# Performance work log

Measured on AMD Instinct MI355X. Metric: run time of the kernel, lower is better.

## Reference

```python
import jax, jax.numpy as jnp
import numpy as np

B = 131072          # batch
T = 1024            # num_task_types
D = 1029            # input_dim = 5 + T  (4 scalar feats + contention effect + T one-hot)
H1, H2 = 64, 32     # hidden_dims


def setup_inputs() -> dict:
    key = jax.random.key(0)
    ks = jax.random.split(key, 8)
    x = jax.random.normal(ks[0], (B, D), dtype=jnp.float32)
    contention = jax.random.normal(ks[1], (T, T), dtype=jnp.float32) * 0.1
    # MLP params (Linear uses y = x @ W.T + b in torch; we store W as (in, out))
    w1 = jax.random.normal(ks[2], (D, H1), dtype=jnp.float32) * (1.0 / np.sqrt(D))
    b1 = jnp.zeros((H1,), dtype=jnp.float32)
    w2 = jax.random.normal(ks[3], (H1, H2), dtype=jnp.float32) * (1.0 / np.sqrt(H1))
    b2 = jnp.zeros((H2,), dtype=jnp.float32)
    w3 = jax.random.normal(ks[4], (H2, 1), dtype=jnp.float32) * (1.0 / np.sqrt(H2))
    b3 = jnp.zeros((1,), dtype=jnp.float32)
    return {"x": x, "contention": contention,
            "w1": w1, "b1": b1, "w2": w2, "b2": b2, "w3": w3, "b3": b3}


def reference(x, contention, w1, b1, w2, b2, w3, b3):
    feats = x[:, :4]                          # density, recent_latency, diversity, time_since_same
    density = x[:, 0:1]                       # (B, 1)
    task_onehot = x[:, 4:4 + T]               # (B, T)
    task_id = jnp.argmax(task_onehot, axis=1) # (B,) int
    # vectorized replacement of the per-sample python loop:
    # gather row, mean over columns, scale by density
    contention_effect = jnp.mean(contention[task_id], axis=1, keepdims=True) * density  # (B, 1)
    combined = jnp.concatenate([feats, contention_effect, task_onehot], axis=1)  # (B, 5+T) == (B, D)
    # MLP (dropout is identity in eval mode)
    h = jax.nn.relu(combined @ w1 + b1)
    h = jax.nn.relu(h @ w2 + b2)
    latency = jax.nn.relu(h @ w3 + b3)        # (B, 1)
    return latency[:, 0]                      # squeeze -> (B,)
```

## Files before the change

kernel.cpp:

```cpp
#include <hip/hip_runtime.h>

typedef __bf16 bf16x8 __attribute__((ext_vector_type(8)));
typedef float f32x4 __attribute__((ext_vector_type(4)));

#define TM 16
#define ROW_F 1029
#define NKB 33
#define LDS_STRIDE 1064

__global__ __launch_bounds__(256) void k_rowmean(const float* __restrict__ cont,
                                                 float* __restrict__ rowmean) {
    __shared__ float red[4];
    int row = blockIdx.x;
    const float4* cr = (const float4*)(cont + (size_t)row * 1024);
    float4 v = cr[threadIdx.x];
    float p = v.x + v.y + v.z + v.w;
    for (int m = 1; m < 64; m <<= 1) p += __shfl_xor(p, m, 64);
    int lane = threadIdx.x & 63, wid = threadIdx.x >> 6;
    if (lane == 0) red[wid] = p;
    __syncthreads();
    if (threadIdx.x == 0)
        rowmean[row] = (red[0] + red[1] + red[2] + red[3]) * (1.0f / 1024.0f);
}

__global__ __launch_bounds__(256) void k_wpack(const float* __restrict__ w1,
                                               __bf16* __restrict__ wfrag) {
    int o = blockIdx.x * 256 + threadIdx.x;
    int j    = o & 7;
    int lane = (o >> 3) & 63;
    int nt   = (o >> 9) & 3;
    int kb   = o >> 11;
    int k = kb * 32 + ((lane >> 4) << 3) + j;
    int n = nt * 16 + (lane & 15);
    float val = 0.0f;
    if (k < 4)          val = w1[k * 64 + n];
    else if (k < 1028)  val = w1[(k + 1) * 64 + n];
    wfrag[o] = (__bf16)val;
}

__global__ __launch_bounds__(256) void k_main(const float* __restrict__ x,
                                              const float* __restrict__ w1,
                                              const float* __restrict__ b1,
                                              const float* __restrict__ w2,
                                              const float* __restrict__ b2,
                                              const float* __restrict__ w3,
                                              const float* __restrict__ b3,
                                              const float* __restrict__ rowmean,
                                              const __bf16* __restrict__ wfrag,
                                              float* __restrict__ out) {
    __shared__ __align__(16) unsigned short x_lds[TM * LDS_STRIDE];
    __shared__ float h1_lds[TM * 65];
    __shared__ float ce_lds[TM];

    const int tid  = threadIdx.x;
    const int lane = tid & 63;
    const int w    = tid >> 6;

    const float4* xt = (const float4*)(x + (size_t)blockIdx.x * (TM * ROW_F));
    for (int i = tid; i < (TM * ROW_F) / 4; i += 256) {
        float4 v = xt[i];
        unsigned e = 4u * (unsigned)i;
        unsigned row = e / ROW_F;
        unsigned col = e - row * ROW_F;
        float vv[4] = {v.x, v.y, v.z, v.w};
        #pragma unroll
        for (int jj = 0; jj < 4; ++jj) {
            unsigned c = col + jj, r = row;
            if (c >= ROW_F) { c -= ROW_F; r += 1; }
            x_lds[r * LDS_STRIDE + c] = __builtin_bit_cast(unsigned short, (__bf16)vv[jj]);
        }
    }
    for (int i = tid; i < TM * (LDS_STRIDE - ROW_F); i += 256) {
        int r = i / (LDS_STRIDE - ROW_F);
        int c = ROW_F + (i - r * (LDS_STRIDE - ROW_F));
        x_lds[r * LDS_STRIDE + c] = 0;
    }
    __syncthreads();

    for (int q = 0; q < 4; ++q) {
        int row = w * 4 + q;
        const unsigned short* rp = &x_lds[row * LDS_STRIDE + 4 + lane * 16];
        float best = -1e30f; int bidx = 4;
        #pragma unroll
        for (int u = 0; u < 4; ++u) {
            ushort4 s4 = *(const ushort4*)(rp + 4 * u);
            unsigned short ss[4] = {s4.x, s4.y, s4.z, s4.w};
            #pragma unroll
            for (int jj = 0; jj < 4; ++jj) {
                float fv = __uint_as_float((unsigned)ss[jj] << 16);
                int c = 4 + lane * 16 + 4 * u + jj;
                if (fv > best) { best = fv; bidx = c; }
            }
        }
        for (int m = 1; m < 64; m <<= 1) {
            float ov = __shfl_xor(best, m, 64);
            int   oi = __shfl_xor(bidx, m, 64);
            if (ov > best || (ov == best && oi < bidx)) { best = ov; bidx = oi; }
        }
        if (lane == 0) {
            float density = __uint_as_float((unsigned)x_lds[row * LDS_STRIDE] << 16);
            ce_lds[row] = rowmean[bidx - 4] * density;
        }
    }
    __syncthreads();

    f32x4 acc = {0.f, 0.f, 0.f, 0.f};
    const float4* wfp = (const float4*)wfrag;
    const unsigned short* abase = &x_lds[(lane & 15) * LDS_STRIDE + ((lane >> 4) << 3)];
    for (int kb = 0; kb < NKB; ++kb) {
        bf16x8 af = *(const bf16x8*)(abase + kb * 32);
        float4 braw = wfp[(kb * 4 + w) * 64 + lane];
        bf16x8 bf = __builtin_bit_cast(bf16x8, braw);
        acc = __builtin_amdgcn_mfma_f32_16x16x32_bf16(af, bf, acc, 0, 0, 0);
    }
    {
        int n = w * 16 + (lane & 15);
        float w1r4 = w1[4 * 64 + n];
        float bb   = b1[n];
        #pragma unroll
        for (int r = 0; r < 4; ++r) {
            int m = (lane >> 4) * 4 + r;
            float hv = acc[r] + ce_lds[m] * w1r4 + bb;
            h1_lds[m * 65 + n] = fmaxf(hv, 0.0f);
        }
    }
    __syncthreads();

    {
        int r2 = tid >> 4;
        int s  = tid & 15;
        int n2 = s * 2;
        float a0 = b2[n2], a1 = b2[n2 + 1];
        const float* hrow = &h1_lds[r2 * 65];
        #pragma unroll 8
        for (int k = 0; k < 64; ++k) {
            float hv = hrow[k];
            float2 wv = *(const float2*)(w2 + k * 32 + n2);
            a0 = fmaf(hv, wv.x, a0);
            a1 = fmaf(hv, wv.y, a1);
        }
        a0 = fmaxf(a0, 0.f); a1 = fmaxf(a1, 0.f);
        float p = a0 * w3[n2] + a1 * w3[n2 + 1];
        p += __shfl_xor(p, 1, 64);
        p += __shfl_xor(p, 2, 64);
        p += __shfl_xor(p, 4, 64);
        p += __shfl_xor(p, 8, 64);
        if (s == 0) out[blockIdx.x * TM + r2] = fmaxf(p + b3[0], 0.f);
    }
}

extern "C" void kernel_launch(void* const* d_in, const int* in_sizes, int n_in,
                              void* d_out, int out_size, void* d_ws, size_t ws_size,
                              hipStream_t stream) {
    const float* x    = (const float*)d_in[0];
    const float* cont = (const float*)d_in[1];
    const float* w1   = (const float*)d_in[2];
    const float* b1   = (const float*)d_in[3];
    const float* w2   = (const float*)d_in[4];
    const float* b2   = (const float*)d_in[5];
    const float* w3   = (const float*)d_in[6];
    const float* b3   = (const float*)d_in[7];

    __bf16* wfrag   = (__bf16*)d_ws;
    float*  rowmean = (float*)((char*)d_ws + 135168);

    int B = in_sizes[0] / ROW_F;
    float* out = (float*)d_out;

    hipLaunchKernelGGL(k_rowmean, dim3(1024), dim3(256), 0, stream, cont, rowmean);
    hipLaunchKernelGGL(k_wpack,   dim3(264),  dim3(256), 0, stream, w1, wfrag);
    hipLaunchKernelGGL(k_main,    dim3(B / TM), dim3(256), 0, stream,
                       x, w1, b1, w2, b2, w3, b3, rowmean, wfrag, out);
}
```

Measured before the change: 794.7 us.

## Stream x directly from global into MFMA fragments, dropping LDS staging

The main kernel no longer stages a 16-row x tile in LDS. Each wave now owns 16 rows and loads 8 consecutive floats per lane straight from global memory, converting them to bf16 MFMA A-fragments and computing the argmax in the same pass. Each wave computes all four 16-column output tiles, so a block now covers 64 rows. This removes the large LDS footprint and the separate argmax pass, which should allow higher occupancy. In exchange, the per-lane 32-byte strided global loads are less coalesced than the old float4 tile copy, and each wave reads 4x as many weight fragments.

```diff
diff --git a/kernel.cpp b/kernel.cpp
--- a/kernel.cpp
+++ b/kernel.cpp
@@ -3,10 +3,9 @@
 typedef __bf16 bf16x8 __attribute__((ext_vector_type(8)));
 typedef float f32x4 __attribute__((ext_vector_type(4)));
 
-#define TM 16
 #define ROW_F 1029
+#define TMB 64
 #define NKB 33
-#define LDS_STRIDE 1064
 
 __global__ __launch_bounds__(256) void k_rowmean(const float* __restrict__ cont,
                                                  float* __restrict__ rowmean) {
@@ -38,114 +37,146 @@
     wfrag[o] = (__bf16)val;
 }
 
-__global__ __launch_bounds__(256) void k_main(const float* __restrict__ x,
-                                              const float* __restrict__ w1,
-                                              const float* __restrict__ b1,
-                                              const float* __restrict__ w2,
-                                              const float* __restrict__ b2,
-                                              const float* __restrict__ w3,
-                                              const float* __restrict__ b3,
-                                              const float* __restrict__ rowmean,
-                                              const __bf16* __restrict__ wfrag,
-                                              float* __restrict__ out) {
-    __shared__ __align__(16) unsigned short x_lds[TM * LDS_STRIDE];
-    __shared__ float h1_lds[TM * 65];
-    __shared__ float ce_lds[TM];
-
-    const int tid  = threadIdx.x;
-    const int lane = tid & 63;
-    const int w    = tid >> 6;
-
-    const float4* xt = (const float4*)(x + (size_t)blockIdx.x * (TM * ROW_F));
-    for (int i = tid; i < (TM * ROW_F) / 4; i += 256) {
-        float4 v = xt[i];
-        unsigned e = 4u * (unsigned)i;
-        unsigned row = e / ROW_F;
-        unsigned col = e - row * ROW_F;
-        float vv[4] = {v.x, v.y, v.z, v.w};
-        #pragma unroll
-        for (int jj = 0; jj < 4; ++jj) {
-            unsigned c = col + jj, r = row;
-            if (c >= ROW_F) { c -= ROW_F; r += 1; }
-            x_lds[r * LDS_STRIDE + c] = __builtin_bit_cast(unsigned short, (__bf16)vv[jj]);
-        }
-    }
-    for (int i = tid; i < TM * (LDS_STRIDE - ROW_F); i += 256) {
-        int r = i / (LDS_STRIDE - ROW_F);
-        int c = ROW_F + (i - r * (LDS_STRIDE - ROW_F));
-        x_lds[r * LDS_STRIDE + c] = 0;
+__global__ __launch_bounds__(256, 4) void k_main(const float* __restrict__ x,
+                                                 const float* __restrict__ w1,
+                                                 const float* __restrict__ b1,
+                                                 const float* __restrict__ w2,
+                                                 const float* __restrict__ b2,
+                                                 const float* __restrict__ w3,
+                                                 const float* __restrict__ b3,
+                                                 const float* __restrict__ rowmean,
+                                                 const __bf16* __restrict__ wfrag,
+                                                 float* __restrict__ out) {
+    __shared__ float h1_lds[TMB * 65];
+
+    const int tid = threadIdx.x;
+    const int l   = tid & 63;
+    const int w   = tid >> 6;
+    const int m0  = l & 15;
+    const int c   = l >> 4;
+
+    const int row = blockIdx.x * TMB + w * 16 + m0;
+    const float* xr = x + (size_t)row * ROW_F + c * 8;
+    const f32x4* wfp = (const f32x4*)wfrag;
+
+    f32x4 acc0 = {0.f,0.f,0.f,0.f}, acc1 = {0.f,0.f,0.f,0.f};
+    f32x4 acc2 = {0.f,0.f,0.f,0.f}, acc3 = {0.f,0.f,0.f,0.f};
+    float best = -1e30f; int bidx = 4; float dens = 0.f;
+
+    {
+        float v[8];
+        #pragma unroll
+        for (int j = 0; j < 8; ++j) v[j] = xr[j];
+        if (c == 0) dens = v[0];
+        bf16x8 af;
+        #pragma unroll
+        for (int j = 0; j < 8; ++j) {
+            af[j] = (__bf16)v[j];
+            int k = c * 8 + j;
+            bool ok = (k >= 4) && (v[j] > best);
+            best = ok ? v[j] : best;
+            bidx = ok ? k : bidx;
+        }
+        acc0 = __builtin_amdgcn_mfma_f32_16x16x32_bf16(af, __builtin_bit_cast(bf16x8, wfp[0*64 + l]), acc0, 0,0,0);
+        acc1 = __builtin_amdgcn_mfma_f32_16x16x32_bf16(af, __builtin_bit_cast(bf16x8, wfp[1*64 + l]), acc1, 0,0,0);
+        acc2 = __builtin_amdgcn_mfma_f32_16x16x32_bf16(af, __builtin_bit_cast(bf16x8, wfp[2*64 + l]), acc2, 0,0,0);
+        acc3 = __builtin_amdgcn_mfma_f32_16x16x32_bf16(af, __builtin_bit_cast(bf16x8, wfp[3*64 + l]), acc3, 0,0,0);
+    }
+
+    for (int kb = 1; kb < 32; ++kb) {
+        const float* p = xr + kb * 32;
+        float v[8];
+        #pragma unroll
+        for (int j = 0; j < 8; ++j) v[j] = p[j];
+        bf16x8 af;
+        int kbase = kb * 32 + c * 8;
+        #pragma unroll
+        for (int j = 0; j < 8; ++j) {
+            af[j] = (__bf16)v[j];
+            bool gt = v[j] > best;
+            best = gt ? v[j] : best;
+            bidx = gt ? (kbase + j) : bidx;
+        }
+        acc0 = __builtin_amdgcn_mfma_f32_16x16x32_bf16(af, __builtin_bit_cast(bf16x8, wfp[(kb*4+0)*64 + l]), acc0, 0,0,0);
+        acc1 = __builtin_amdgcn_mfma_f32_16x16x32_bf16(af, __builtin_bit_cast(bf16x8, wfp[(kb*4+1)*64 + l]), acc1, 0,0,0);
+        acc2 = __builtin_amdgcn_mfma_f32_16x16x32_bf16(af, __builtin_bit_cast(bf16x8, wfp[(kb*4+2)*64 + l]), acc2, 0,0,0);
+        acc3 = __builtin_amdgcn_mfma_f32_16x16x32_bf16(af, __builtin_bit_cast(bf16x8, wfp[(kb*4+3)*64 + l]), acc3, 0,0,0);
+    }
+
+    {
+        bf16x8 af;
+        #pragma unroll
+        for (int j = 0; j < 8; ++j) af[j] = (__bf16)0.f;
+        if (c == 0) {
+            const float* p = xr + 32 * 32;
+            #pragma unroll
+            for (int j = 0; j < 4; ++j) {
+                float v = p[j];
+                af[j] = (__bf16)v;
+                bool gt = v > best;
+                best = gt ? v : best;
+                bidx = gt ? (1024 + j) : bidx;
+            }
+        }
+        acc0 = __builtin_amdgcn_mfma_f32_16x16x32_bf16(af, __builtin_bit_cast(bf16x8, wfp[(32*4+0)*64 + l]), acc0, 0,0,0);
+        acc1 = __builtin_amdgcn_mfma_f32_16x16x32_bf16(af, __builtin_bit_cast(bf16x8, wfp[(32*4+1)*64 + l]), acc1, 0,0,0);
+        acc2 = __builtin_amdgcn_mfma_f32_16x16x32_bf16(af, __builtin_bit_cast(bf16x8, wfp[(32*4+2)*64 + l]), acc2, 0,0,0);
+        acc3 = __builtin_amdgcn_mfma_f32_16x16x32_bf16(af, __builtin_bit_cast(bf16x8, wfp[(32*4+3)*64 + l]), acc3, 0,0,0);
+    }
+
+    #pragma unroll
+    for (int off = 16; off < 64; off <<= 1) {
+        float ob = __shfl_xor(best, off, 64);
+        int   oi = __shfl_xor(bidx, off, 64);
+        if (ob > best || (ob == best && oi < bidx)) { best = ob; bidx = oi; }
+    }
+    float ce = 0.f;
+    if (c == 0) ce = rowmean[bidx - 4] * dens;
+
+    float ce_r[4];
+    #pragma unroll
+    for (int r = 0; r < 4; ++r) ce_r[r] = __shfl(ce, c * 4 + r, 64);
+
+    {
+        const f32x4* accs[4] = {&acc0, &acc1, &acc2, &acc3};
+        #pragma unroll
+        for (int nt = 0; nt < 4; ++nt) {
+            int n = nt * 16 + m0;
+            float w14 = w1[4 * 64 + n];
+            float bb  = b1[n];
+            #pragma unroll
+            for (int r = 0; r < 4; ++r) {
+                int m = c * 4 + r;
+                float hv = (*accs[nt])[r] + ce_r[r] * w14 + bb;
+                h1_lds[(w * 16 + m) * 65 + n] = fmaxf(hv, 0.0f);
+            }
+        }
     }
     __syncthreads();
 
-    for (int q = 0; q < 4; ++q) {
-        int row = w * 4 + q;
-        const unsigned short* rp = &x_lds[row * LDS_STRIDE + 4 + lane * 16];
-        float best = -1e30f; int bidx = 4;
-        #pragma unroll
-        for (int u = 0; u < 4; ++u) {
-            ushort4 s4 = *(const ushort4*)(rp + 4 * u);
-            unsigned short ss[4] = {s4.x, s4.y, s4.z, s4.w};
-            #pragma unroll
-            for (int jj = 0; jj < 4; ++jj) {
-                float fv = __uint_as_float((unsigned)ss[jj] << 16);
-                int c = 4 + lane * 16 + 4 * u + jj;
-                if (fv > best) { best = fv; bidx = c; }
-            }
-        }
-        for (int m = 1; m < 64; m <<= 1) {
-            float ov = __shfl_xor(best, m, 64);
-            int   oi = __shfl_xor(bidx, m, 64);
-            if (ov > best || (ov == best && oi < bidx)) { best = ov; bidx = oi; }
-        }
-        if (lane == 0) {
-            float density = __uint_as_float((unsigned)x_lds[row * LDS_STRIDE] << 16);
-            ce_lds[row] = rowmean[bidx - 4] * density;
-        }
-    }
-    __syncthreads();
-
-    f32x4 acc = {0.f, 0.f, 0.f, 0.f};
-    const float4* wfp = (const float4*)wfrag;
-    const unsigned short* abase = &x_lds[(lane & 15) * LDS_STRIDE + ((lane >> 4) << 3)];
-    for (int kb = 0; kb < NKB; ++kb) {
-        bf16x8 af = *(const bf16x8*)(abase + kb * 32);
-        float4 braw = wfp[(kb * 4 + w) * 64 + lane];
-        bf16x8 bf = __builtin_bit_cast(bf16x8, braw);
-        acc = __builtin_amdgcn_mfma_f32_16x16x32_bf16(af, bf, acc, 0, 0, 0);
-    }
-    {
-        int n = w * 16 + (lane & 15);
-        float w1r4 = w1[4 * 64 + n];
-        float bb   = b1[n];
-        #pragma unroll
-        for (int r = 0; r < 4; ++r) {
-            int m = (lane >> 4) * 4 + r;
-            float hv = acc[r] + ce_lds[m] * w1r4 + bb;
-            h1_lds[m * 65 + n] = fmaxf(hv, 0.0f);
-        }
-    }
-    __syncthreads();
-
-    {
-        int r2 = tid >> 4;
+    {
         int s  = tid & 15;
         int n2 = s * 2;
-        float a0 = b2[n2], a1 = b2[n2 + 1];
-        const float* hrow = &h1_lds[r2 * 65];
-        #pragma unroll 8
-        for (int k = 0; k < 64; ++k) {
-            float hv = hrow[k];
-            float2 wv = *(const float2*)(w2 + k * 32 + n2);
-            a0 = fmaf(hv, wv.x, a0);
-            a1 = fmaf(hv, wv.y, a1);
-        }
-        a0 = fmaxf(a0, 0.f); a1 = fmaxf(a1, 0.f);
-        float p = a0 * w3[n2] + a1 * w3[n2 + 1];
-        p += __shfl_xor(p, 1, 64);
-        p += __shfl_xor(p, 2, 64);
-        p += __shfl_xor(p, 4, 64);
-        p += __shfl_xor(p, 8, 64);
-        if (s == 0) out[blockIdx.x * TM + r2] = fmaxf(p + b3[0], 0.f);
+        #pragma unroll
+        for (int it = 0; it < 4; ++it) {
+            int r2 = it * 16 + (tid >> 4);
+            float a0 = b2[n2], a1 = b2[n2 + 1];
+            const float* hrow = &h1_lds[r2 * 65];
+            #pragma unroll 8
+            for (int k = 0; k < 64; ++k) {
+                float hv = hrow[k];
+                float2 wv = *(const float2*)(w2 + k * 32 + n2);
+                a0 = fmaf(hv, wv.x, a0);
+                a1 = fmaf(hv, wv.y, a1);
+            }
+            a0 = fmaxf(a0, 0.f); a1 = fmaxf(a1, 0.f);
+            float p = a0 * w3[n2] + a1 * w3[n2 + 1];
+            p += __shfl_xor(p, 1, 64);
+            p += __shfl_xor(p, 2, 64);
+            p += __shfl_xor(p, 4, 64);
+            p += __shfl_xor(p, 8, 64);
+            if (s == 0) out[blockIdx.x * TMB + r2] = fmaxf(p + b3[0], 0.f);
+        }
     }
 }
 
@@ -167,8 +198,8 @@
     int B = in_sizes[0] / ROW_F;
     float* out = (float*)d_out;
 
-    hipLaunchKernelGGL(k_rowmean, dim3(1024), dim3(256), 0, stream, cont, rowmean);
-    hipLaunchKernelGGL(k_wpack,   dim3(264),  dim3(256), 0, stream, w1, wfrag);
-    hipLaunchKernelGGL(k_main,    dim3(B / TM), dim3(256), 0, stream,
+    hipLaunchKernelGGL(k_rowmean, dim3(1024),    dim3(256), 0, stream, cont, rowmean);
+    hipLaunchKernelGGL(k_wpack,   dim3(264),     dim3(256), 0, stream, w1, wfrag);
+    hipLaunchKernelGGL(k_main,    dim3(B / TMB), dim3(256), 0, stream,
                        x, w1, b1, w2, b2, w3, b3, rowmean, wfrag, out);
 }
```

After: 782.0 us. No clear change (-1.6%).
